# Performance work log

Hardware: AMD Instinct MI355X
Metric: run time of the kernel (lower is better)

Reference implementation:

```python
import jax, jax.numpy as jnp
import numpy as np

LN_EPS = 1e-5

def _layernorm(x, g, b):
    m = jnp.mean(x, axis=-1, keepdims=True)
    v = jnp.var(x, axis=-1, keepdims=True)
    return (x - m) / jnp.sqrt(v + LN_EPS) * g + b

def setup_inputs() -> dict:
    key = jax.random.key(0)
    ks = jax.random.split(key, 16)
    N, E, D, P = 25000, 500000, 256, 64  # nodes, edges, node_dim, pair_dim
    def rn(k, shape, scale=1.0):
        return jax.random.normal(k, shape, dtype=jnp.float32) * scale
    return {
        "x": rn(ks[0], (N, D)),
        "rbf_r": rn(ks[1], (E, P)),
        "factor_r": jax.random.uniform(ks[2], (E, 1), dtype=jnp.float32),
        "sph_v0": rn(ks[3], (E, 5, 1)),  # l=2 spherical harmonics (5 comps)
        "sph_v1": rn(ks[4], (E, 3, 1)),  # l=1 spherical harmonics (3 comps)
        "W_down": rn(ks[5], (D, P), D ** -0.5),
        "b_down": jnp.zeros((P,), jnp.float32),
        "W_up0": rn(ks[6], (P, 2 * P), P ** -0.5),
        "b_up0": jnp.zeros((2 * P,), jnp.float32),
        "W_up1": rn(ks[7], (P, 2 * P), P ** -0.5),
        "W_uph": rn(ks[8], (P, 2 * P), P ** -0.5),
        "W_n1": rn(ks[9], (6 * P, D), (6 * P) ** -0.5),
        "b_n1": jnp.zeros((D,), jnp.float32),
        "ln_g": jnp.ones((D,), jnp.float32),
        "ln_b": jnp.zeros((D,), jnp.float32),
        "W_n2": rn(ks[10], (D, D), D ** -0.5),
        "b_n2": jnp.zeros((D,), jnp.float32),
        "j": jax.random.randint(ks[11], (E,), 0, N, dtype=jnp.int32),
        "i": jax.random.randint(ks[12], (E,), 0, N, dtype=jnp.int32),
    }

def reference(x, rbf_r, factor_r, sph_v0, sph_v1, W_down, b_down, W_up0, b_up0,
              W_up1, W_uph, W_n1, b_n1, ln_g, ln_b, W_n2, b_n2, j, i):
    N = x.shape[0]
    _x = x @ W_down + b_down                      # [N, P]
    l0_pair = _x[j] * rbf_r * factor_r            # [E, P]
    agg0 = jax.ops.segment_sum(l0_pair, i, num_segments=N)                     # [N, P]
    agg1 = jax.ops.segment_sum(l0_pair[:, None, :] * sph_v1, i, num_segments=N)  # [N, 3, P]
    aggh = jax.ops.segment_sum(l0_pair[:, None, :] * sph_v0, i, num_segments=N)  # [N, 5, P]
    l0_node = (_x * agg0) @ W_up0 + b_up0                                      # [N, 2P]
    l1_node = jnp.sum(jnp.square((_x[:, None, :] * agg1) @ W_up1), axis=1)     # [N, 2P]
    lh_node = jnp.sum(jnp.square((_x[:, None, :] * aggh) @ W_uph), axis=1)     # [N, 2P]
    node = jnp.concatenate([l0_node, l1_node, lh_node], axis=-1)               # [N, 6P]
    h = jax.nn.silu(_layernorm(node @ W_n1 + b_n1, ln_g, ln_b))
    return h @ W_n2 + b_n2 + x  # dropout is identity in eval
```

## Files before the change

### kernel.cpp

```cpp
#include <hip/hip_runtime.h>
#include <hip/hip_bf16.h>

typedef __attribute__((ext_vector_type(8))) short bf16x8;
typedef __attribute__((ext_vector_type(4))) float f32x4;

__device__ __forceinline__ unsigned short f2bf(float f) {
    unsigned u = __float_as_uint(f);
    return (unsigned short)((u + 0x7FFF + ((u >> 16) & 1)) >> 16);
}
__device__ __forceinline__ unsigned pack2(float a, float b) {
    return (unsigned)f2bf(a) | ((unsigned)f2bf(b) << 16);
}
__device__ __forceinline__ float ubf(unsigned short h) {
    return __uint_as_float((unsigned)h << 16);
}
__device__ __forceinline__ int RLi(float v, int k) {
    return __builtin_amdgcn_readlane(__float_as_int(v), k);
}
__device__ __forceinline__ float RLf(float v, int k) {
    return __uint_as_float((unsigned)__builtin_amdgcn_readlane(__float_as_int(v), k));
}

__device__ void swz_body(const float* __restrict__ W,
                         unsigned short* __restrict__ Bsw, int K, int idx)
{
    int total = (K >> 5) * 1024;
    if (idx >= total) return;
    int lane = idx & 63;
    int ct = (idx >> 6) & 15;
    int ks = idx >> 10;
    int col = ct * 16 + (lane & 15);
    int kbase = (ks << 5) + ((lane >> 4) << 3);
    const float* p = &W[(size_t)kbase * 256 + col];
    uint4 o;
    o.x = pack2(p[0 * 256], p[1 * 256]);
    o.y = pack2(p[2 * 256], p[3 * 256]);
    o.z = pack2(p[4 * 256], p[5 * 256]);
    o.w = pack2(p[6 * 256], p[7 * 256]);
    *(uint4*)&Bsw[(size_t)idx * 8] = o;
}

__device__ void swz_split_body(const float* __restrict__ W,
                               unsigned short* __restrict__ Bh,
                               unsigned short* __restrict__ Bl,
                               int K, int C, int idx)
{
    int ct_n = C >> 4;
    int total = (K >> 5) * ct_n * 64;
    if (idx >= total) return;
    int per_ks = ct_n * 64;
    int ks = idx / per_ks;
    int rem = idx - ks * per_ks;
    int ct = rem >> 6;
    int lane = rem & 63;
    int col = ct * 16 + (lane & 15);
    int kbase = (ks << 5) + ((lane >> 4) << 3);
    const float* p = &W[(size_t)kbase * C + col];
    unsigned short hs[8], ls[8];
#pragma unroll
    for (int j = 0; j < 8; j++) {
        float wv = p[(size_t)j * C];
        unsigned short h = f2bf(wv);
        hs[j] = h;
        ls[j] = f2bf(wv - ubf(h));
    }
    uint4 oh, ol;
    oh.x = (unsigned)hs[0] | ((unsigned)hs[1] << 16);
    oh.y = (unsigned)hs[2] | ((unsigned)hs[3] << 16);
    oh.z = (unsigned)hs[4] | ((unsigned)hs[5] << 16);
    oh.w = (unsigned)hs[6] | ((unsigned)hs[7] << 16);
    ol.x = (unsigned)ls[0] | ((unsigned)ls[1] << 16);
    ol.y = (unsigned)ls[2] | ((unsigned)ls[3] << 16);
    ol.z = (unsigned)ls[4] | ((unsigned)ls[5] << 16);
    ol.w = (unsigned)ls[6] | ((unsigned)ls[7] << 16);
    *(uint4*)&Bh[(size_t)idx * 8] = oh;
    *(uint4*)&Bl[(size_t)idx * 8] = ol;
}

__global__ __launch_bounds__(256) void k_prep(
    const float* __restrict__ Wn1, unsigned short* __restrict__ Bsw1,
    const float* __restrict__ Wn2, unsigned short* __restrict__ Bsw2,
    const float* __restrict__ Wu0, unsigned short* __restrict__ Wu0h, unsigned short* __restrict__ Wu0l,
    const float* __restrict__ Wu1, unsigned short* __restrict__ Wu1h, unsigned short* __restrict__ Wu1l,
    const float* __restrict__ Wuh, unsigned short* __restrict__ Wuhh, unsigned short* __restrict__ Wuhl,
    const float* __restrict__ Wd, unsigned short* __restrict__ Wdh, unsigned short* __restrict__ Wdl,
    int* __restrict__ counts, int N)
{
    int b = blockIdx.x;
    int tid = threadIdx.x;
    if (b < 48)       swz_body(Wn1, Bsw1, 384, b * 256 + tid);
    else if (b < 80)  swz_body(Wn2, Bsw2, 256, (b - 48) * 256 + tid);
    else if (b < 84)  swz_split_body(Wu0, Wu0h, Wu0l, 64, 128, (b - 80) * 256 + tid);
    else if (b < 88)  swz_split_body(Wu1, Wu1h, Wu1l, 64, 128, (b - 84) * 256 + tid);
    else if (b < 92)  swz_split_body(Wuh, Wuhh, Wuhl, 64, 128, (b - 88) * 256 + tid);
    else if (b < 100) swz_split_body(Wd, Wdh, Wdl, 256, 64, (b - 92) * 256 + tid);
    else {
        for (int i = (b - 100) * 256 + tid; i < N + 1; i += 25 * 256)
            counts[i] = 0;
    }
}

__global__ __launch_bounds__(256, 4) void k_down_hist(
    const float* __restrict__ x, const unsigned short* __restrict__ Wdh,
    const unsigned short* __restrict__ Wdl, const float* __restrict__ bd,
    float* __restrict__ xp, const int* __restrict__ iidx,
    int* __restrict__ counts, int N, int E, int nDown)
{
    __shared__ __align__(16) unsigned short Ahi[32 * 264];
    __shared__ __align__(16) unsigned short Alo[32 * 264];

    if ((int)blockIdx.x >= nDown) {
        int e = ((int)blockIdx.x - nDown) * 256 + threadIdx.x;
        if (e < E) atomicAdd(&counts[iidx[e]], 1);
        return;
    }

    int n0 = blockIdx.x * 32;
    int tid = threadIdx.x;
    int lane = tid & 63;
    int w = tid >> 6;
    int rt = w & 1;
    int cg = w >> 1;
    int lcol = lane & 15;
    int quad = lane >> 4;
    int kq = quad * 8;

    for (int t = tid; t < 32 * 64; t += 256) {
        int r = t >> 6, c4 = t & 63;
        int n = n0 + r;
        float4 v = {0.f, 0.f, 0.f, 0.f};
        if (n < N) v = *(const float4*)&x[(size_t)n * 256 + c4 * 4];
        unsigned short hx = f2bf(v.x), hy = f2bf(v.y);
        unsigned short hz = f2bf(v.z), hw = f2bf(v.w);
        uint2 oh, ol;
        oh.x = (unsigned)hx | ((unsigned)hy << 16);
        oh.y = (unsigned)hz | ((unsigned)hw << 16);
        ol.x = (unsigned)f2bf(v.x - ubf(hx)) | ((unsigned)f2bf(v.y - ubf(hy)) << 16);
        ol.y = (unsigned)f2bf(v.z - ubf(hz)) | ((unsigned)f2bf(v.w - ubf(hw)) << 16);
        *(uint2*)&Ahi[r * 264 + c4 * 4] = oh;
        *(uint2*)&Alo[r * 264 + c4 * 4] = ol;
    }
    __syncthreads();

    int arow = rt * 16 + lcol;
    f32x4 acc[2];
    acc[0] = (f32x4){0.f, 0.f, 0.f, 0.f};
    acc[1] = (f32x4){0.f, 0.f, 0.f, 0.f};
#pragma unroll
    for (int ks = 0; ks < 8; ks++) {
        bf16x8 ah = *(const bf16x8*)&Ahi[arow * 264 + ks * 32 + kq];
        bf16x8 al = *(const bf16x8*)&Alo[arow * 264 + ks * 32 + kq];
#pragma unroll
        for (int t = 0; t < 2; t++) {
            int ct = cg * 2 + t;
            size_t bi = ((size_t)((ks * 4 + ct) * 64 + lane)) * 8;
            bf16x8 bh = *(const bf16x8*)&Wdh[bi];
            bf16x8 bl = *(const bf16x8*)&Wdl[bi];
            acc[t] = __builtin_amdgcn_mfma_f32_16x16x32_bf16(ah, bh, acc[t], 0, 0, 0);
            acc[t] = __builtin_amdgcn_mfma_f32_16x16x32_bf16(ah, bl, acc[t], 0, 0, 0);
            acc[t] = __builtin_amdgcn_mfma_f32_16x16x32_bf16(al, bh, acc[t], 0, 0, 0);
        }
    }
#pragma unroll
    for (int t = 0; t < 2; t++) {
        int col = cg * 32 + t * 16 + lcol;
        float bb = bd[col];
#pragma unroll
        for (int q = 0; q < 4; q++) {
            int row = rt * 16 + quad * 4 + q;
            int n = n0 + row;
            if (n < N) xp[(size_t)n * 64 + col] = acc[t][q] + bb;
        }
    }
}

__global__ __launch_bounds__(1024) void k_scan(
    const int* __restrict__ counts, int* __restrict__ rowptr,
    int* __restrict__ cursor, int N)
{
    __shared__ int part[1024];
    int t = threadIdx.x;
    int chunk = (N + 1023) / 1024;
    int beg = t * chunk;
    int end = min(beg + chunk, N);
    int s = 0;
    for (int i = beg; i < end; i++) s += counts[i];
    part[t] = s;
    __syncthreads();
    for (int off = 1; off < 1024; off <<= 1) {
        int v = (t >= off) ? part[t - off] : 0;
        __syncthreads();
        part[t] += v;
        __syncthreads();
    }
    int run = (t == 0) ? 0 : part[t - 1];
    for (int i = beg; i < end; i++) {
        rowptr[i] = run;
        cursor[i] = run;
        run += counts[i];
    }
    if (t == 1023) rowptr[N] = part[1023];
}

__global__ __launch_bounds__(256) void k_scatter_pack(
    const int* __restrict__ iidx, const int* __restrict__ jidx,
    const float* __restrict__ factor, const float* __restrict__ sph0,
    const float* __restrict__ sph1, int* __restrict__ cursor,
    float* __restrict__ packed, int E)
{
    int e = blockIdx.x * 256 + threadIdx.x;
    if (e >= E) return;
    int pos = atomicAdd(&cursor[iidx[e]], 1);
    float4 w0, w1, w2;
    w0.x = __int_as_float(e);
    w0.y = __int_as_float(jidx[e]);
    w0.z = factor[e];
    w0.w = sph1[e * 3 + 0];
    w1.x = sph1[e * 3 + 1];
    w1.y = sph1[e * 3 + 2];
    w1.z = sph0[e * 5 + 0];
    w1.w = sph0[e * 5 + 1];
    w2.x = sph0[e * 5 + 2];
    w2.y = sph0[e * 5 + 3];
    w2.z = sph0[e * 5 + 4];
    w2.w = 0.f;
    float4* q = (float4*)&packed[(size_t)pos * 12];
    q[0] = w0; q[1] = w1; q[2] = w2;
}

__global__ __launch_bounds__(256) void k_gather(
    const float* __restrict__ xp, const float* __restrict__ rbf,
    const float* __restrict__ packed, const int* __restrict__ rowptr,
    float* __restrict__ agg0, float* __restrict__ agg1,
    float* __restrict__ aggh, int N)
{
    int n = blockIdx.x * 4 + (threadIdx.x >> 6);
    if (n >= N) return;
    int p = threadIdx.x & 63;
    int beg = rowptr[n], end = rowptr[n + 1];

    float a0 = 0.f;
    float a1x = 0.f, a1y = 0.f, a1z = 0.f;
    float h0 = 0.f, h1 = 0.f, h2 = 0.f, h3 = 0.f, h4 = 0.f;

    for (int base = beg; base < end; base += 64) {
        int m = end - base;
        if (m > 64) m = 64;
        float4 w0 = {0.f, 0.f, 0.f, 0.f};
        float4 w1 = {0.f, 0.f, 0.f, 0.f};
        float4 w2 = {0.f, 0.f, 0.f, 0.f};
        if (base + p < end) {
            const float4* q = (const float4*)&packed[(size_t)(base + p) * 12];
            w0 = q[0]; w1 = q[1]; w2 = q[2];
        }
        int k = 0;
        for (; k + 3 < m; k += 4) {
            int e0 = RLi(w0.x, k),     e1 = RLi(w0.x, k + 1);
            int e2 = RLi(w0.x, k + 2), e3 = RLi(w0.x, k + 3);
            int j0 = RLi(w0.y, k),     j1 = RLi(w0.y, k + 1);
            int j2 = RLi(w0.y, k + 2), j3 = RLi(w0.y, k + 3);
            float x0 = xp[(size_t)j0 * 64 + p], r0 = rbf[(size_t)e0 * 64 + p];
            float x1 = xp[(size_t)j1 * 64 + p], r1 = rbf[(size_t)e1 * 64 + p];
            float x2 = xp[(size_t)j2 * 64 + p], r2 = rbf[(size_t)e2 * 64 + p];
            float x3 = xp[(size_t)j3 * 64 + p], r3 = rbf[(size_t)e3 * 64 + p];
            float f0 = RLf(w0.z, k),     f1 = RLf(w0.z, k + 1);
            float f2 = RLf(w0.z, k + 2), f3 = RLf(w0.z, k + 3);
            float v0 = x0 * r0 * f0, v1 = x1 * r1 * f1;
            float v2 = x2 * r2 * f2, v3 = x3 * r3 * f3;
            a0 += (v0 + v1) + (v2 + v3);
            a1x += v0 * RLf(w0.w, k)     + v1 * RLf(w0.w, k + 1)
                 + v2 * RLf(w0.w, k + 2) + v3 * RLf(w0.w, k + 3);
            a1y += v0 * RLf(w1.x, k)     + v1 * RLf(w1.x, k + 1)
                 + v2 * RLf(w1.x, k + 2) + v3 * RLf(w1.x, k + 3);
            a1z += v0 * RLf(w1.y, k)     + v1 * RLf(w1.y, k + 1)
                 + v2 * RLf(w1.y, k + 2) + v3 * RLf(w1.y, k + 3);
            h0  += v0 * RLf(w1.z, k)     + v1 * RLf(w1.z, k + 1)
                 + v2 * RLf(w1.z, k + 2) + v3 * RLf(w1.z, k + 3);
            h1  += v0 * RLf(w1.w, k)     + v1 * RLf(w1.w, k + 1)
                 + v2 * RLf(w1.w, k + 2) + v3 * RLf(w1.w, k + 3);
            h2  += v0 * RLf(w2.x, k)     + v1 * RLf(w2.x, k + 1)
                 + v2 * RLf(w2.x, k + 2) + v3 * RLf(w2.x, k + 3);
            h3  += v0 * RLf(w2.y, k)     + v1 * RLf(w2.y, k + 1)
                 + v2 * RLf(w2.y, k + 2) + v3 * RLf(w2.y, k + 3);
            h4  += v0 * RLf(w2.z, k)     + v1 * RLf(w2.z, k + 1)
                 + v2 * RLf(w2.z, k + 2) + v3 * RLf(w2.z, k + 3);
        }
        for (; k < m; k++) {
            int e0 = RLi(w0.x, k);
            int j0 = RLi(w0.y, k);
            float f0 = RLf(w0.z, k);
            float v0 = xp[(size_t)j0 * 64 + p] * rbf[(size_t)e0 * 64 + p] * f0;
            a0 += v0;
            a1x += v0 * RLf(w0.w, k);
            a1y += v0 * RLf(w1.x, k);
            a1z += v0 * RLf(w1.y, k);
            h0  += v0 * RLf(w1.z, k);
            h1  += v0 * RLf(w1.w, k);
            h2  += v0 * RLf(w2.x, k);
            h3  += v0 * RLf(w2.y, k);
            h4  += v0 * RLf(w2.z, k);
        }
    }

    agg0[(size_t)n * 64 + p] = a0;
    agg1[((size_t)n * 3 + 0) * 64 + p] = a1x;
    agg1[((size_t)n * 3 + 1) * 64 + p] = a1y;
    agg1[((size_t)n * 3 + 2) * 64 + p] = a1z;
    aggh[((size_t)n * 5 + 0) * 64 + p] = h0;
    aggh[((size_t)n * 5 + 1) * 64 + p] = h1;
    aggh[((size_t)n * 5 + 2) * 64 + p] = h2;
    aggh[((size_t)n * 5 + 3) * 64 + p] = h3;
    aggh[((size_t)n * 5 + 4) * 64 + p] = h4;
}

__global__ __launch_bounds__(256, 3) void k_node(
    const float* __restrict__ xp, const float* __restrict__ agg0,
    const float* __restrict__ agg1, const float* __restrict__ aggh,
    const unsigned short* __restrict__ Wu0h, const unsigned short* __restrict__ Wu0l,
    const unsigned short* __restrict__ Wu1h, const unsigned short* __restrict__ Wu1l,
    const unsigned short* __restrict__ Wuhh, const unsigned short* __restrict__ Wuhl,
    const float* __restrict__ bu0, unsigned short* __restrict__ node, int N)
{
    __shared__ float xs[16 * 64];
    __shared__ __align__(16) unsigned short Ahi[9 * 16 * 72];
    __shared__ __align__(16) unsigned short Alo[9 * 16 * 72];

    int n0 = blockIdx.x * 16;
    int tid = threadIdx.x;
    int lane = tid & 63;
    int w = tid >> 6;
    int lcol = lane & 15;
    int quad = lane >> 4;
    int kq = quad * 8;

    for (int t = tid; t < 16 * 64; t += 256) {
        int n = n0 + (t >> 6);
        xs[t] = (n < N) ? xp[(size_t)n * 64 + (t & 63)] : 0.f;
    }
    __syncthreads();

    for (int t = tid; t < 9 * 1024; t += 256) {
        int m = t >> 10;
        int rem = t & 1023;
        int r = rem >> 6, c = rem & 63;
        int n = n0 + r;
        float v = 0.f;
        if (n < N) {
            float xv = xs[rem];
            if (m == 0)      v = xv * agg0[(size_t)n * 64 + c];
            else if (m < 4)  v = xv * agg1[((size_t)n * 3 + (m - 1)) * 64 + c];
            else             v = xv * aggh[((size_t)n * 5 + (m - 4)) * 64 + c];
        }
        unsigned short h = f2bf(v);
        float fh = __uint_as_float((unsigned)h << 16);
        Ahi[(m * 16 + r) * 72 + c] = h;
        Alo[(m * 16 + r) * 72 + c] = f2bf(v - fh);
    }
    __syncthreads();

    {
        bf16x8 bh[2][2], bl[2][2];
#pragma unroll
        for (int ks = 0; ks < 2; ks++)
#pragma unroll
            for (int t = 0; t < 2; t++) {
                size_t bi = ((size_t)((ks * 8 + w * 2 + t) * 64 + lane)) * 8;
                bh[ks][t] = *(const bf16x8*)&Wu0h[bi];
                bl[ks][t] = *(const bf16x8*)&Wu0l[bi];
            }
        f32x4 acc[2];
        acc[0] = (f32x4){0.f, 0.f, 0.f, 0.f};
        acc[1] = (f32x4){0.f, 0.f, 0.f, 0.f};
#pragma unroll
        for (int ks = 0; ks < 2; ks++) {
            bf16x8 ah = *(const bf16x8*)&Ahi[lcol * 72 + ks * 32 + kq];
            bf16x8 al = *(const bf16x8*)&Alo[lcol * 72 + ks * 32 + kq];
#pragma unroll
            for (int t = 0; t < 2; t++) {
                acc[t] = __builtin_amdgcn_mfma_f32_16x16x32_bf16(ah, bh[ks][t], acc[t], 0, 0, 0);
                acc[t] = __builtin_amdgcn_mfma_f32_16x16x32_bf16(ah, bl[ks][t], acc[t], 0, 0, 0);
                acc[t] = __builtin_amdgcn_mfma_f32_16x16x32_bf16(al, bh[ks][t], acc[t], 0, 0, 0);
            }
        }
#pragma unroll
        for (int t = 0; t < 2; t++) {
            int col = w * 32 + t * 16 + lcol;
            float bb = bu0[col];
#pragma unroll
            for (int q = 0; q < 4; q++) {
                int n = n0 + quad * 4 + q;
                if (n < N) node[(size_t)n * 384 + col] = f2bf(acc[t][q] + bb);
            }
        }
    }

    {
        bf16x8 bh[2][2], bl[2][2];
#pragma unroll
        for (int ks = 0; ks < 2; ks++)
#pragma unroll
            for (int t = 0; t < 2; t++) {
                size_t bi = ((size_t)((ks * 8 + w * 2 + t) * 64 + lane)) * 8;
                bh[ks][t] = *(const bf16x8*)&Wu1h[bi];
                bl[ks][t] = *(const bf16x8*)&Wu1l[bi];
            }
        f32x4 S[2];
        S[0] = (f32x4){0.f, 0.f, 0.f, 0.f};
        S[1] = (f32x4){0.f, 0.f, 0.f, 0.f};
#pragma unroll
        for (int c = 0; c < 3; c++) {
            f32x4 d[2];
            d[0] = (f32x4){0.f, 0.f, 0.f, 0.f};
            d[1] = (f32x4){0.f, 0.f, 0.f, 0.f};
            int abase = (1 + c) * (16 * 72);
#pragma unroll
            for (int ks = 0; ks < 2; ks++) {
                bf16x8 ah = *(const bf16x8*)&Ahi[abase + lcol * 72 + ks * 32 + kq];
                bf16x8 al = *(const bf16x8*)&Alo[abase + lcol * 72 + ks * 32 + kq];
#pragma unroll
                for (int t = 0; t < 2; t++) {
                    d[t] = __builtin_amdgcn_mfma_f32_16x16x32_bf16(ah, bh[ks][t], d[t], 0, 0, 0);
                    d[t] = __builtin_amdgcn_mfma_f32_16x16x32_bf16(ah, bl[ks][t], d[t], 0, 0, 0);
                    d[t] = __builtin_amdgcn_mfma_f32_16x16x32_bf16(al, bh[ks][t], d[t], 0, 0, 0);
                }
            }
            S[0] += d[0] * d[0];
            S[1] += d[1] * d[1];
        }
#pragma unroll
        for (int t = 0; t < 2; t++) {
            int col = w * 32 + t * 16 + lcol;
#pragma unroll
            for (int q = 0; q < 4; q++) {
                int n = n0 + quad * 4 + q;
                if (n < N) node[(size_t)n * 384 + 128 + col] = f2bf(S[t][q]);
            }
        }
    }

    {
        bf16x8 bh[2][2], bl[2][2];
#pragma unroll
        for (int ks = 0; ks < 2; ks++)
#pragma unroll
            for (int t = 0; t < 2; t++) {
                size_t bi = ((size_t)((ks * 8 + w * 2 + t) * 64 + lane)) * 8;
                bh[ks][t] = *(const bf16x8*)&Wuhh[bi];
                bl[ks][t] = *(const bf16x8*)&Wuhl[bi];
            }
        f32x4 S[2];
        S[0] = (f32x4){0.f, 0.f, 0.f, 0.f};
        S[1] = (f32x4){0.f, 0.f, 0.f, 0.f};
#pragma unroll
        for (int c = 0; c < 5; c++) {
            f32x4 d[2];
            d[0] = (f32x4){0.f, 0.f, 0.f, 0.f};
            d[1] = (f32x4){0.f, 0.f, 0.f, 0.f};
            int abase = (4 + c) * (16 * 72);
#pragma unroll
            for (int ks = 0; ks < 2; ks++) {
                bf16x8 ah = *(const bf16x8*)&Ahi[abase + lcol * 72 + ks * 32 + kq];
                bf16x8 al = *(const bf16x8*)&Alo[abase + lcol * 72 + ks * 32 + kq];
#pragma unroll
                for (int t = 0; t < 2; t++) {
                    d[t] = __builtin_amdgcn_mfma_f32_16x16x32_bf16(ah, bh[ks][t], d[t], 0, 0, 0);
                    d[t] = __builtin_amdgcn_mfma_f32_16x16x32_bf16(ah, bl[ks][t], d[t], 0, 0, 0);
                    d[t] = __builtin_amdgcn_mfma_f32_16x16x32_bf16(al, bh[ks][t], d[t], 0, 0, 0);
                }
            }
            S[0] += d[0] * d[0];
            S[1] += d[1] * d[1];
        }
#pragma unroll
        for (int t = 0; t < 2; t++) {
            int col = w * 32 + t * 16 + lcol;
#pragma unroll
            for (int q = 0; q < 4; q++) {
                int n = n0 + quad * 4 + q;
                if (n < N) node[(size_t)n * 384 + 256 + col] = f2bf(S[t][q]);
            }
        }
    }
}

__global__ __launch_bounds__(256, 4) void k_final(
    const unsigned short* __restrict__ node, const unsigned short* __restrict__ Bsw1,
    const float* __restrict__ bn1, const float* __restrict__ lng,
    const float* __restrict__ lnb, const unsigned short* __restrict__ Bsw2,
    const float* __restrict__ bn2, const float* __restrict__ x,
    float* __restrict__ out, int N)
{
    __shared__ __align__(16) unsigned short Abf[32 * 392];
    __shared__ float red[32][33];
    __shared__ float red2[32][33];
    __shared__ float mstat[32][2];

    int n0 = blockIdx.x * 32;
    int tid = threadIdx.x;
    int lane = tid & 63;
    int w = tid >> 6;
    int rt = w & 1;
    int cg = w >> 1;
    int lcol = lane & 15;
    int quad = lane >> 4;
    int arow = rt * 16 + lcol;
    int kq = quad * 8;

    for (int i = tid; i < 32 * 48; i += 256) {
        int r = i / 48, c8 = i - r * 48;
        int n = n0 + r;
        uint4 v = {0u, 0u, 0u, 0u};
        if (n < N) v = *(const uint4*)&node[(size_t)n * 384 + c8 * 8];
        *(uint4*)&Abf[r * 392 + c8 * 8] = v;
    }
    __syncthreads();

    f32x4 acc[8];
#pragma unroll
    for (int t = 0; t < 8; t++) acc[t] = (f32x4){0.f, 0.f, 0.f, 0.f};
    for (int ks = 0; ks < 12; ks++) {
        bf16x8 a = *(const bf16x8*)&Abf[arow * 392 + ks * 32 + kq];
        const bf16x8* bp =
            (const bf16x8*)&Bsw1[(size_t)(((ks * 16 + cg * 8) * 64) + lane) * 8];
#pragma unroll
        for (int t = 0; t < 8; t++)
            acc[t] = __builtin_amdgcn_mfma_f32_16x16x32_bf16(a, bp[t * 64], acc[t], 0, 0, 0);
    }

    float bias[8];
#pragma unroll
    for (int t = 0; t < 8; t++) bias[t] = bn1[cg * 128 + t * 16 + lcol];
#pragma unroll
    for (int q = 0; q < 4; q++) {
        float s = 0.f, s2 = 0.f;
#pragma unroll
        for (int t = 0; t < 8; t++) {
            float v = acc[t][q] + bias[t];
            s += v; s2 += v * v;
        }
        int row = rt * 16 + quad * 4 + q;
        red[row][cg * 16 + lcol] = s;
        red2[row][cg * 16 + lcol] = s2;
    }
    __syncthreads();
    if (tid < 32) {
        float s = 0.f, s2 = 0.f;
#pragma unroll
        for (int u = 0; u < 32; u++) { s += red[tid][u]; s2 += red2[tid][u]; }
        float m = s * (1.f / 256.f);
        float var = s2 * (1.f / 256.f) - m * m;
        mstat[tid][0] = m;
        mstat[tid][1] = rsqrtf(var + 1e-5f);
    }
    __syncthreads();

#pragma unroll
    for (int t = 0; t < 8; t++) {
        int col = cg * 128 + t * 16 + lcol;
        float gg = lng[col], bb = lnb[col];
#pragma unroll
        for (int q = 0; q < 4; q++) {
            int row = rt * 16 + quad * 4 + q;
            float z = (acc[t][q] + bias[t] - mstat[row][0]) * mstat[row][1] * gg + bb;
            float h = z / (1.f + __expf(-z));
            Abf[row * 264 + col] = f2bf(h);
        }
    }
    __syncthreads();

    f32x4 o[8];
#pragma unroll
    for (int t = 0; t < 8; t++) o[t] = (f32x4){0.f, 0.f, 0.f, 0.f};
    for (int ks = 0; ks < 8; ks++) {
        bf16x8 a = *(const bf16x8*)&Abf[arow * 264 + ks * 32 + kq];
        const bf16x8* bp =
            (const bf16x8*)&Bsw2[(size_t)(((ks * 16 + cg * 8) * 64) + lane) * 8];
#pragma unroll
        for (int t = 0; t < 8; t++)
            o[t] = __builtin_amdgcn_mfma_f32_16x16x32_bf16(a, bp[t * 64], o[t], 0, 0, 0);
    }
#pragma unroll
    for (int t = 0; t < 8; t++) {
        int col = cg * 128 + t * 16 + lcol;
        float ob = bn2[col];
#pragma unroll
        for (int q = 0; q < 4; q++) {
            int row = rt * 16 + quad * 4 + q;
            int n = n0 + row;
            if (n < N)
                out[(size_t)n * 256 + col] = o[t][q] + ob + x[(size_t)n * 256 + col];
        }
    }
}

extern "C" void kernel_launch(void* const* d_in, const int* in_sizes, int n_in,
                              void* d_out, int out_size, void* d_ws, size_t ws_size,
                              hipStream_t stream)
{
    const float* x      = (const float*)d_in[0];
    const float* rbf    = (const float*)d_in[1];
    const float* factor = (const float*)d_in[2];
    const float* sph0   = (const float*)d_in[3];
    const float* sph1   = (const float*)d_in[4];
    const float* Wd     = (const float*)d_in[5];
    const float* bd     = (const float*)d_in[6];
    const float* Wu0    = (const float*)d_in[7];
    const float* bu0    = (const float*)d_in[8];
    const float* Wu1    = (const float*)d_in[9];
    const float* Wuh    = (const float*)d_in[10];
    const float* Wn1    = (const float*)d_in[11];
    const float* bn1    = (const float*)d_in[12];
    const float* lng    = (const float*)d_in[13];
    const float* lnb    = (const float*)d_in[14];
    const float* Wn2    = (const float*)d_in[15];
    const float* bn2    = (const float*)d_in[16];
    const int*   jidx   = (const int*)d_in[17];
    const int*   iidx   = (const int*)d_in[18];
    float* out = (float*)d_out;

    int N = in_sizes[0] / 256;
    int E = in_sizes[17];

    float* ws   = (float*)d_ws;
    float* xp   = ws;
    float* agg0 = xp   + (size_t)N * 64;
    float* agg1 = agg0 + (size_t)N * 64;
    float* aggh = agg1 + (size_t)N * 192;
    float* nodeF = aggh + (size_t)N * 320;
    unsigned short* nodeB = (unsigned short*)nodeF;
    unsigned short* Bsw1 = (unsigned short*)(nodeF + (size_t)N * 384);
    unsigned short* Bsw2 = Bsw1 + 12 * 16 * 64 * 8;
    unsigned short* Wu0h_s = Bsw2 + 8 * 16 * 64 * 8;
    unsigned short* Wu0l_s = Wu0h_s + 64 * 128;
    unsigned short* Wu1h_s = Wu0l_s + 64 * 128;
    unsigned short* Wu1l_s = Wu1h_s + 64 * 128;
    unsigned short* Wuhh_s = Wu1l_s + 64 * 128;
    unsigned short* Wuhl_s = Wuhh_s + 64 * 128;
    unsigned short* Wdh_s  = Wuhl_s + 64 * 128;
    unsigned short* Wdl_s  = Wdh_s + 256 * 64;

    int* counts  = (int*)nodeF;
    int* rowptr  = counts + (N + 1);
    int* cursor  = rowptr + (N + 1);
    float* packed = nodeF + 131072;

    int nDown = (N + 31) / 32;
    int nHist = (E + 255) / 256;

    k_prep<<<dim3(125), dim3(256), 0, stream>>>(
        Wn1, Bsw1, Wn2, Bsw2, Wu0, Wu0h_s, Wu0l_s, Wu1, Wu1h_s, Wu1l_s,
        Wuh, Wuhh_s, Wuhl_s, Wd, Wdh_s, Wdl_s, counts, N);
    k_down_hist<<<dim3(nDown + nHist), dim3(256), 0, stream>>>(
        x, Wdh_s, Wdl_s, bd, xp, iidx, counts, N, E, nDown);
    k_scan<<<dim3(1), dim3(1024), 0, stream>>>(counts, rowptr, cursor, N);
    k_scatter_pack<<<dim3(nHist), dim3(256), 0, stream>>>(
        iidx, jidx, factor, sph0, sph1, cursor, packed, E);
    k_gather<<<dim3((N + 3) / 4), dim3(256), 0, stream>>>(
        xp, rbf, packed, rowptr, agg0, agg1, aggh, N);
    k_node<<<dim3((N + 15) / 16), dim3(256), 0, stream>>>(
        xp, agg0, agg1, aggh, Wu0h_s, Wu0l_s, Wu1h_s, Wu1l_s, Wuhh_s, Wuhl_s,
        bu0, nodeB, N);
    k_final<<<dim3((N + 31) / 32), dim3(256), 0, stream>>>(
        nodeB, Bsw1, bn1, lng, lnb, Bsw2, bn2, x, out, N);
}
```

Measured before the change: 478.5 us.

## Fuse x-multiply and bf16 hi/lo split into gather epilogue, tile-major layout

The gather kernel now multiplies each aggregate by the node's projected x and splits it into bf16 hi/lo parts itself. It writes them in a 16-node tile-major layout that matches the node kernel's shared-memory A tiles. The node kernel then only does 16-byte vector copies into LDS and no longer reloads x or does the fp32 conversion. This removes some fp32 intermediate traffic, since 2x bf16 is the same bytes as fp32, and simplifies node-kernel staging. In exchange, the gather kernel's stores become 2-byte scattered writes.

```diff
diff --git a/kernel.cpp b/kernel.cpp
--- a/kernel.cpp
+++ b/kernel.cpp
@@ -231,8 +231,8 @@
 __global__ __launch_bounds__(256) void k_gather(
     const float* __restrict__ xp, const float* __restrict__ rbf,
     const float* __restrict__ packed, const int* __restrict__ rowptr,
-    float* __restrict__ agg0, float* __restrict__ agg1,
-    float* __restrict__ aggh, int N)
+    unsigned short* __restrict__ aggHi, unsigned short* __restrict__ aggLo,
+    int N)
 {
     int n = blockIdx.x * 4 + (threadIdx.x >> 6);
     if (n >= N) return;
@@ -302,26 +302,25 @@
         }
     }
 
-    agg0[(size_t)n * 64 + p] = a0;
-    agg1[((size_t)n * 3 + 0) * 64 + p] = a1x;
-    agg1[((size_t)n * 3 + 1) * 64 + p] = a1y;
-    agg1[((size_t)n * 3 + 2) * 64 + p] = a1z;
-    aggh[((size_t)n * 5 + 0) * 64 + p] = h0;
-    aggh[((size_t)n * 5 + 1) * 64 + p] = h1;
-    aggh[((size_t)n * 5 + 2) * 64 + p] = h2;
-    aggh[((size_t)n * 5 + 3) * 64 + p] = h3;
-    aggh[((size_t)n * 5 + 4) * 64 + p] = h4;
+    float xv = xp[(size_t)n * 64 + p];
+    float vals[9] = {xv * a0, xv * a1x, xv * a1y, xv * a1z,
+                     xv * h0, xv * h1, xv * h2, xv * h3, xv * h4};
+    size_t b9 = (size_t)(n >> 4) * 9216 + (size_t)(n & 15) * 64 + p;
+#pragma unroll
+    for (int m = 0; m < 9; m++) {
+        unsigned short hh = f2bf(vals[m]);
+        aggHi[b9 + m * 1024] = hh;
+        aggLo[b9 + m * 1024] = f2bf(vals[m] - ubf(hh));
+    }
 }
 
 __global__ __launch_bounds__(256, 3) void k_node(
-    const float* __restrict__ xp, const float* __restrict__ agg0,
-    const float* __restrict__ agg1, const float* __restrict__ aggh,
+    const unsigned short* __restrict__ aggHi, const unsigned short* __restrict__ aggLo,
     const unsigned short* __restrict__ Wu0h, const unsigned short* __restrict__ Wu0l,
     const unsigned short* __restrict__ Wu1h, const unsigned short* __restrict__ Wu1l,
     const unsigned short* __restrict__ Wuhh, const unsigned short* __restrict__ Wuhl,
     const float* __restrict__ bu0, unsigned short* __restrict__ node, int N)
 {
-    __shared__ float xs[16 * 64];
     __shared__ __align__(16) unsigned short Ahi[9 * 16 * 72];
     __shared__ __align__(16) unsigned short Alo[9 * 16 * 72];
 
@@ -333,28 +332,20 @@
     int quad = lane >> 4;
     int kq = quad * 8;
 
-    for (int t = tid; t < 16 * 64; t += 256) {
-        int n = n0 + (t >> 6);
-        xs[t] = (n < N) ? xp[(size_t)n * 64 + (t & 63)] : 0.f;
-    }
-    __syncthreads();
-
-    for (int t = tid; t < 9 * 1024; t += 256) {
-        int m = t >> 10;
-        int rem = t & 1023;
-        int r = rem >> 6, c = rem & 63;
-        int n = n0 + r;
-        float v = 0.f;
-        if (n < N) {
-            float xv = xs[rem];
-            if (m == 0)      v = xv * agg0[(size_t)n * 64 + c];
-            else if (m < 4)  v = xv * agg1[((size_t)n * 3 + (m - 1)) * 64 + c];
-            else             v = xv * aggh[((size_t)n * 5 + (m - 4)) * 64 + c];
-        }
-        unsigned short h = f2bf(v);
-        float fh = __uint_as_float((unsigned)h << 16);
-        Ahi[(m * 16 + r) * 72 + c] = h;
-        Alo[(m * 16 + r) * 72 + c] = f2bf(v - fh);
+    size_t gbase = (size_t)blockIdx.x * 9216;
+    for (int t = tid; t < 1152; t += 256) {
+        int row = t >> 3, c8 = t & 7;
+        int n = n0 + (row & 15);
+        uint4 v = {0u, 0u, 0u, 0u};
+        if (n < N) v = *(const uint4*)&aggHi[gbase + (size_t)row * 64 + c8 * 8];
+        *(uint4*)&Ahi[row * 72 + c8 * 8] = v;
+    }
+    for (int t = tid; t < 1152; t += 256) {
+        int row = t >> 3, c8 = t & 7;
+        int n = n0 + (row & 15);
+        uint4 v = {0u, 0u, 0u, 0u};
+        if (n < N) v = *(const uint4*)&aggLo[gbase + (size_t)row * 64 + c8 * 8];
+        *(uint4*)&Alo[row * 72 + c8 * 8] = v;
     }
     __syncthreads();
 
@@ -620,13 +611,14 @@
 
     int N = in_sizes[0] / 256;
     int E = in_sizes[17];
+    int nblk = (N + 15) / 16;
 
     float* ws   = (float*)d_ws;
     float* xp   = ws;
-    float* agg0 = xp   + (size_t)N * 64;
-    float* agg1 = agg0 + (size_t)N * 64;
-    float* aggh = agg1 + (size_t)N * 192;
-    float* nodeF = aggh + (size_t)N * 320;
+    float* aggF = xp + (size_t)N * 64;
+    unsigned short* aggHi = (unsigned short*)aggF;
+    unsigned short* aggLo = aggHi + (size_t)nblk * 9216;
+    float* nodeF = aggF + (size_t)nblk * 9216;
     unsigned short* nodeB = (unsigned short*)nodeF;
     unsigned short* Bsw1 = (unsigned short*)(nodeF + (size_t)N * 384);
     unsigned short* Bsw2 = Bsw1 + 12 * 16 * 64 * 8;
@@ -656,9 +648,9 @@
     k_scatter_pack<<<dim3(nHist), dim3(256), 0, stream>>>(
         iidx, jidx, factor, sph0, sph1, cursor, packed, E);
     k_gather<<<dim3((N + 3) / 4), dim3(256), 0, stream>>>(
-        xp, rbf, packed, rowptr, agg0, agg1, aggh, N);
-    k_node<<<dim3((N + 15) / 16), dim3(256), 0, stream>>>(
-        xp, agg0, agg1, aggh, Wu0h_s, Wu0l_s, Wu1h_s, Wu1l_s, Wuhh_s, Wuhl_s,
+        xp, rbf, packed, rowptr, aggHi, aggLo, N);
+    k_node<<<dim3(nblk), dim3(256), 0, stream>>>(
+        aggHi, aggLo, Wu0h_s, Wu0l_s, Wu1h_s, Wu1l_s, Wuhh_s, Wuhl_s,
         bu0, nodeB, N);
     k_final<<<dim3((N + 31) / 32), dim3(256), 0, stream>>>(
         nodeB, Bsw1, bn1, lng, lnb, Bsw2, bn2, x, out, N);
```

After: 449.9 us. 6.0% less time.
